# Kernel optimization log

Measured on AMD Instinct MI355X. Metric: run time of the kernel, lower is better.

## Reference

```python
import jax, jax.numpy as jnp
import numpy as np

HIDDEN = 768
HEADS = 12


def setup_inputs() -> dict:
    key = jax.random.key(0)
    ks = jax.random.split(key, 9)
    B, T, C = 2, 4096, HIDDEN
    s = 1.0 / np.sqrt(C)
    x = jax.random.normal(ks[0], (B, T, C), dtype=jnp.float32)
    Wq = jax.random.normal(ks[1], (C, C), dtype=jnp.float32) * s
    bq = jnp.zeros((C,), dtype=jnp.float32)
    Wk = jax.random.normal(ks[2], (C, C), dtype=jnp.float32) * s
    bk = jnp.zeros((C,), dtype=jnp.float32)
    Wv = jax.random.normal(ks[3], (C, C), dtype=jnp.float32) * s
    bv = jnp.zeros((C,), dtype=jnp.float32)
    Wo = jax.random.normal(ks[4], (C, C), dtype=jnp.float32) * s
    bo = jnp.zeros((C,), dtype=jnp.float32)
    return {"x": x, "Wq": Wq, "bq": bq, "Wk": Wk, "bk": bk,
            "Wv": Wv, "bv": bv, "Wo": Wo, "bo": bo}


def reference(x, Wq, bq, Wk, bk, Wv, bv, Wo, bo):
    B, T, C = x.shape
    H = HEADS
    D = C // H
    # projections -> [B, H, T, D]
    def split_heads(y):
        return y.reshape(B, T, H, D).transpose(0, 2, 1, 3)
    q = split_heads(x @ Wq + bq)
    k = split_heads(x @ Wk + bk)
    v = split_heads(x @ Wv + bv)
    # scores [B, H, T, T], scaled by 1/sqrt(D)
    scores = jnp.einsum('bhqd,bhkd->bhqk', q, k) / jnp.sqrt(jnp.asarray(D, x.dtype))
    causal = jnp.tril(jnp.ones((T, T), dtype=bool))
    scores = jnp.where(causal[None, None], scores, jnp.asarray(-jnp.inf, x.dtype))
    weights = jax.nn.softmax(scores, axis=-1)
    # dropout_prob = 0.0 (eval-equivalent), so dropouts are identity
    out = jnp.einsum('bhqk,bhkd->bhqd', weights, v)  # [B,H,T,D]
    out = out.transpose(0, 2, 1, 3).reshape(B, T, C)
    return out @ Wo + bo
```

## Files before the change

kernel.cpp:

```cpp
#include <hip/hip_runtime.h>

typedef unsigned short ushort_t;
typedef __bf16 bf16x8 __attribute__((ext_vector_type(8)));
typedef float f4v __attribute__((ext_vector_type(4)));

#define B_ 2
#define T_ 4096
#define C_ 768
#define H_ 12
#define D_ 64
#define BT_ (B_*T_)

#define XB_SZ   (BT_*C_*2)
#define WT_SZ   (C_*C_*2)
#define QKV_SZ  (BT_*C_*2)
#define WS_XB   0
#define WS_WT   (WS_XB + XB_SZ)
#define WS_Q    (WS_WT + 4*WT_SZ)
#define WS_K    (WS_Q + QKV_SZ)
#define WS_V    (WS_K + QKV_SZ)
#define WS_AO   (WS_V + QKV_SZ)
#define WS_TOTAL (WS_AO + QKV_SZ)

#define QSCALE  0.18033688f

__device__ __forceinline__ ushort_t f2bf(float f) {
    unsigned u = __float_as_uint(f);
    u += 0x7FFFu + ((u >> 16) & 1u);
    return (ushort_t)(u >> 16);
}

__device__ __forceinline__ void gload16(const void* gsrc, void* ldst) {
    __builtin_amdgcn_global_load_lds(
        (const __attribute__((address_space(1))) unsigned int*)gsrc,
        (__attribute__((address_space(3))) unsigned int*)ldst, 16, 0, 0);
}

__global__ __launch_bounds__(256) void k_convert_x(const float* __restrict__ x,
                                                   ushort_t* __restrict__ xb, int n4) {
    int i = blockIdx.x * 256 + threadIdx.x;
    if (i >= n4) return;
    float4 v = ((const float4*)x)[i];
    ushort4 o;
    o.x = f2bf(v.x); o.y = f2bf(v.y); o.z = f2bf(v.z); o.w = f2bf(v.w);
    ((ushort4*)xb)[i] = o;
}

__global__ __launch_bounds__(256) void k_wt(const float* __restrict__ w0,
                                            const float* __restrict__ w1,
                                            const float* __restrict__ w2,
                                            const float* __restrict__ w3,
                                            ushort_t* __restrict__ wt) {
    __shared__ float tile[32][33];
    int wi = blockIdx.z;
    const float* W = (wi == 0) ? w0 : (wi == 1) ? w1 : (wi == 2) ? w2 : w3;
    ushort_t* out = wt + wi * C_ * C_;
    int k0 = blockIdx.x * 32, n0 = blockIdx.y * 32;
    int tx = threadIdx.x & 31, ty = threadIdx.x >> 5;
#pragma unroll
    for (int i = 0; i < 4; ++i) {
        int kr = ty * 4 + i;
        tile[kr][tx] = W[(k0 + kr) * C_ + n0 + tx];
    }
    __syncthreads();
#pragma unroll
    for (int i = 0; i < 4; ++i) {
        int nr = ty * 4 + i;
        out[(n0 + nr) * C_ + k0 + tx] = f2bf(tile[tx][nr]);
    }
}

__global__ __launch_bounds__(256) void k_gemm_qkv(
    const ushort_t* __restrict__ Xb, const ushort_t* __restrict__ WtAll,
    const float* __restrict__ bq, const float* __restrict__ bk, const float* __restrict__ bv,
    ushort_t* __restrict__ Qo, ushort_t* __restrict__ Ko, ushort_t* __restrict__ Vo) {
    __shared__ ushort_t lsA[128 * 64];
    __shared__ ushort_t lsB[128 * 64];
    char* lsAb = (char*)lsA;
    char* lsBb = (char*)lsB;
    const int z = blockIdx.z;
    const ushort_t* Wt = WtAll + z * C_ * C_;
    const float* bias = (z == 0) ? bq : (z == 1) ? bk : bv;
    const int m0 = blockIdx.x * 128, n0 = blockIdx.y * 128;
    const int tid = threadIdx.x;
    const int w = tid >> 6, lane = tid & 63, lg = lane >> 4, lr = lane & 15;
    const int wm = w >> 1, wn = w & 1;
    f4v acc[4][4] = {};
    for (int ks = 0; ks < 12; ++ks) {
        const int k0 = ks * 64;
        __syncthreads();
#pragma unroll
        for (int i = 0; i < 4; ++i) {
            int s = tid + 256 * i;
            int r = s >> 3, cs = (s & 7) ^ (r & 7);
            gload16(Xb + (m0 + r) * C_ + k0 + cs * 8, lsAb + i * 4096 + w * 1024);
            gload16(Wt + (n0 + r) * C_ + k0 + cs * 8, lsBb + i * 4096 + w * 1024);
        }
        __syncthreads();
#pragma unroll
        for (int kk = 0; kk < 2; ++kk) {
            bf16x8 af[4], bfr[4];
            const int kb = (kk * 32 + lg * 8) * 2;
#pragma unroll
            for (int i = 0; i < 4; ++i) {
                int ra = wm * 64 + i * 16 + lr;
                af[i] = *(const bf16x8*)(lsAb + ra * 128 + (kb ^ ((ra & 7) << 4)));
                int rb = wn * 64 + i * 16 + lr;
                bfr[i] = *(const bf16x8*)(lsBb + rb * 128 + (kb ^ ((rb & 7) << 4)));
            }
#pragma unroll
            for (int mi = 0; mi < 4; ++mi)
#pragma unroll
                for (int nj = 0; nj < 4; ++nj)
                    acc[mi][nj] = __builtin_amdgcn_mfma_f32_16x16x32_bf16(af[mi], bfr[nj], acc[mi][nj], 0, 0, 0);
        }
    }
    const float scale = (z == 0) ? QSCALE : 1.0f;
    const int mbase = m0 + wm * 64, nbase = n0 + wn * 64;
    if (z < 2) {
        ushort_t* outp = (z == 0) ? Qo : Ko;
#pragma unroll
        for (int mi = 0; mi < 4; ++mi) {
#pragma unroll
            for (int nj = 0; nj < 4; ++nj) {
                int col = nbase + nj * 16 + lr;
                int h = col >> 6, d = col & 63;
                float bv_ = bias[col];
#pragma unroll
                for (int j = 0; j < 4; ++j) {
                    int m = mbase + mi * 16 + lg * 4 + j;
                    int bb = m >> 12, t = m & 4095;
                    outp[((bb * H_ + h) * T_ + t) * D_ + d] = f2bf((acc[mi][nj][j] + bv_) * scale);
                }
            }
        }
    } else {
#pragma unroll
        for (int mi = 0; mi < 4; ++mi) {
            int m0j = mbase + mi * 16 + lg * 4;
            int bb = m0j >> 12, t0 = m0j & 4095;
#pragma unroll
            for (int nj = 0; nj < 4; ++nj) {
                int col = nbase + nj * 16 + lr;
                int h = col >> 6, d = col & 63;
                float bv_ = bias[col];
                ushort4 pk;
                pk.x = f2bf(acc[mi][nj][0] + bv_);
                pk.y = f2bf(acc[mi][nj][1] + bv_);
                pk.z = f2bf(acc[mi][nj][2] + bv_);
                pk.w = f2bf(acc[mi][nj][3] + bv_);
                *(ushort4*)(Vo + ((size_t)(bb * H_ + h) * D_ + d) * T_ + t0) = pk;
            }
        }
    }
}

__global__ __launch_bounds__(256) void k_flash(const ushort_t* __restrict__ Q,
                                               const ushort_t* __restrict__ K,
                                               const ushort_t* __restrict__ Vt,
                                               ushort_t* __restrict__ AO) {
    __shared__ ushort_t lsK[64 * 64];
    __shared__ ushort_t lsV[64 * 64];
    __shared__ ushort_t lsP[4 * 16 * 64];
    char* lsKb = (char*)lsK;
    char* lsVb = (char*)lsV;
    const int idx = blockIdx.x;
    const int pi = idx / 24;
    const int bh = idx % 24;
    const int b = bh / H_, h = bh % H_;
    const int tid = threadIdx.x, w = tid >> 6, lane = tid & 63, lg = lane >> 4, lr = lane & 15;
    char* lsPb = (char*)(lsP + w * 16 * 64);
    const ushort_t* qb = Q + (size_t)bh * T_ * D_;
    const ushort_t* kb = K + (size_t)bh * T_ * D_;
    const ushort_t* vtb = Vt + (size_t)bh * D_ * T_;
    ushort_t* aob = AO + (size_t)b * T_ * C_ + h * D_;

    for (int half = 0; half < 2; ++half) {
        const int qt = half ? pi : (63 - pi);
        const int q0 = qt * 64;
        const int wave_qmin = q0 + w * 16;
        bf16x8 aq[2];
#pragma unroll
        for (int kk = 0; kk < 2; ++kk)
            aq[kk] = *(const bf16x8*)(qb + (size_t)(wave_qmin + lr) * D_ + kk * 32 + lg * 8);
        float m_s[4], l_s[4];
        f4v o[4] = {};
#pragma unroll
        for (int j = 0; j < 4; ++j) { m_s[j] = -1e30f; l_s[j] = 0.f; }

        const int ntiles = qt + 1;
        for (int kt = 0; kt < ntiles; ++kt) {
            const int kv0 = kt * 64;
            __syncthreads();
#pragma unroll
            for (int i = 0; i < 2; ++i) {
                int s = tid + 256 * i;
                int r = s >> 3, cs = (s & 7) ^ (r & 7);
                gload16(kb + (size_t)(kv0 + r) * D_ + cs * 8, lsKb + i * 4096 + w * 1024);
                gload16(vtb + (size_t)r * T_ + kv0 + cs * 8, lsVb + i * 4096 + w * 1024);
            }
            __syncthreads();
            f4v sf[4] = {};
#pragma unroll
            for (int kk = 0; kk < 2; ++kk) {
                const int kbyte = (kk * 32 + lg * 8) * 2;
                bf16x8 bk_[4];
#pragma unroll
                for (int nt = 0; nt < 4; ++nt) {
                    int rk = nt * 16 + lr;
                    bk_[nt] = *(const bf16x8*)(lsKb + rk * 128 + (kbyte ^ ((rk & 7) << 4)));
                }
                __builtin_amdgcn_s_setprio(1);
#pragma unroll
                for (int nt = 0; nt < 4; ++nt)
                    sf[nt] = __builtin_amdgcn_mfma_f32_16x16x32_bf16(aq[kk], bk_[nt], sf[nt], 0, 0, 0);
                __builtin_amdgcn_s_setprio(0);
            }
            if (kv0 + 63 > wave_qmin) {
#pragma unroll
                for (int nt = 0; nt < 4; ++nt)
#pragma unroll
                    for (int j = 0; j < 4; ++j) {
                        int qg = wave_qmin + lg * 4 + j;
                        int kg = kv0 + nt * 16 + lr;
                        if (kg > qg) sf[nt][j] = -1e30f;
                    }
            }
#pragma unroll
            for (int j = 0; j < 4; ++j) {
                float rm = fmaxf(fmaxf(sf[0][j], sf[1][j]), fmaxf(sf[2][j], sf[3][j]));
                rm = fmaxf(rm, __shfl_xor(rm, 1));
                rm = fmaxf(rm, __shfl_xor(rm, 2));
                rm = fmaxf(rm, __shfl_xor(rm, 4));
                rm = fmaxf(rm, __shfl_xor(rm, 8));
                float mo = m_s[j];
                float mn = fmaxf(mo, rm);
                float alpha = exp2f(mo - mn);
                float rs = 0.f;
                int prow = lg * 4 + j;
#pragma unroll
                for (int nt = 0; nt < 4; ++nt) {
                    float p = exp2f(sf[nt][j] - mn);
                    rs += p;
                    int cbyte = (nt * 16 + lr) * 2;
                    *(ushort_t*)(lsPb + prow * 128 + (cbyte ^ ((prow & 7) << 4))) = f2bf(p);
                }
                rs += __shfl_xor(rs, 1);
                rs += __shfl_xor(rs, 2);
                rs += __shfl_xor(rs, 4);
                rs += __shfl_xor(rs, 8);
                l_s[j] = l_s[j] * alpha + rs;
                m_s[j] = mn;
#pragma unroll
                for (int nt = 0; nt < 4; ++nt) o[nt][j] *= alpha;
            }
#pragma unroll
            for (int kk = 0; kk < 2; ++kk) {
                const int kvbyte = (kk * 32 + lg * 8) * 2;
                bf16x8 ap, bv_[4];
                ap = *(const bf16x8*)(lsPb + lr * 128 + (kvbyte ^ ((lr & 7) << 4)));
#pragma unroll
                for (int nt = 0; nt < 4; ++nt) {
                    int rd = nt * 16 + lr;
                    bv_[nt] = *(const bf16x8*)(lsVb + rd * 128 + (kvbyte ^ ((rd & 7) << 4)));
                }
                __builtin_amdgcn_s_setprio(1);
#pragma unroll
                for (int nt = 0; nt < 4; ++nt)
                    o[nt] = __builtin_amdgcn_mfma_f32_16x16x32_bf16(ap, bv_[nt], o[nt], 0, 0, 0);
                __builtin_amdgcn_s_setprio(0);
            }
        }
#pragma unroll
        for (int j = 0; j < 4; ++j) {
            float inv = 1.f / l_s[j];
            int qg = wave_qmin + lg * 4 + j;
#pragma unroll
            for (int nt = 0; nt < 4; ++nt) {
                int d = nt * 16 + lr;
                aob[(size_t)qg * C_ + d] = f2bf(o[nt][j] * inv);
            }
        }
    }
}

__global__ __launch_bounds__(256) void k_gemm_out(const ushort_t* __restrict__ Ab,
                                                  const ushort_t* __restrict__ Wt,
                                                  const float* __restrict__ bo,
                                                  float* __restrict__ Out) {
    __shared__ ushort_t lsA[128 * 64];
    __shared__ ushort_t lsB[128 * 64];
    char* lsAb = (char*)lsA;
    char* lsBb = (char*)lsB;
    const int m0 = blockIdx.x * 128, n0 = blockIdx.y * 128;
    const int tid = threadIdx.x;
    const int w = tid >> 6, lane = tid & 63, lg = lane >> 4, lr = lane & 15;
    const int wm = w >> 1, wn = w & 1;
    f4v acc[4][4] = {};
    for (int ks = 0; ks < 12; ++ks) {
        const int k0 = ks * 64;
        __syncthreads();
#pragma unroll
        for (int i = 0; i < 4; ++i) {
            int s = tid + 256 * i;
            int r = s >> 3, cs = (s & 7) ^ (r & 7);
            gload16(Ab + (m0 + r) * C_ + k0 + cs * 8, lsAb + i * 4096 + w * 1024);
            gload16(Wt + (n0 + r) * C_ + k0 + cs * 8, lsBb + i * 4096 + w * 1024);
        }
        __syncthreads();
#pragma unroll
        for (int kk = 0; kk < 2; ++kk) {
            bf16x8 af[4], bfr[4];
            const int kb = (kk * 32 + lg * 8) * 2;
#pragma unroll
            for (int i = 0; i < 4; ++i) {
                int ra = wm * 64 + i * 16 + lr;
                af[i] = *(const bf16x8*)(lsAb + ra * 128 + (kb ^ ((ra & 7) << 4)));
                int rb = wn * 64 + i * 16 + lr;
                bfr[i] = *(const bf16x8*)(lsBb + rb * 128 + (kb ^ ((rb & 7) << 4)));
            }
#pragma unroll
            for (int mi = 0; mi < 4; ++mi)
#pragma unroll
                for (int nj = 0; nj < 4; ++nj)
                    acc[mi][nj] = __builtin_amdgcn_mfma_f32_16x16x32_bf16(af[mi], bfr[nj], acc[mi][nj], 0, 0, 0);
        }
    }
    const int mbase = m0 + wm * 64, nbase = n0 + wn * 64;
#pragma unroll
    for (int mi = 0; mi < 4; ++mi) {
#pragma unroll
        for (int nj = 0; nj < 4; ++nj) {
            int col = nbase + nj * 16 + lr;
            float bv_ = bo[col];
#pragma unroll
            for (int j = 0; j < 4; ++j) {
                int m = mbase + mi * 16 + lg * 4 + j;
                Out[(size_t)m * C_ + col] = acc[mi][nj][j] + bv_;
            }
        }
    }
}

extern "C" void kernel_launch(void* const* d_in, const int* in_sizes, int n_in,
                              void* d_out, int out_size, void* d_ws, size_t ws_size,
                              hipStream_t stream) {
    const float* x  = (const float*)d_in[0];
    const float* Wq = (const float*)d_in[1];
    const float* bq = (const float*)d_in[2];
    const float* Wk = (const float*)d_in[3];
    const float* bk = (const float*)d_in[4];
    const float* Wv = (const float*)d_in[5];
    const float* bv = (const float*)d_in[6];
    const float* Wo = (const float*)d_in[7];
    const float* bo = (const float*)d_in[8];
    float* out = (float*)d_out;
    char* ws = (char*)d_ws;
    if (ws_size < (size_t)WS_TOTAL) return;

    ushort_t* Xb = (ushort_t*)(ws + WS_XB);
    ushort_t* Wt = (ushort_t*)(ws + WS_WT);
    ushort_t* Qb = (ushort_t*)(ws + WS_Q);
    ushort_t* Kb = (ushort_t*)(ws + WS_K);
    ushort_t* Vb = (ushort_t*)(ws + WS_V);
    ushort_t* Ao = (ushort_t*)(ws + WS_AO);

    k_convert_x<<<dim3(BT_ * C_ / 4 / 256), 256, 0, stream>>>(x, Xb, BT_ * C_ / 4);
    k_wt<<<dim3(24, 24, 4), 256, 0, stream>>>(Wq, Wk, Wv, Wo, Wt);
    k_gemm_qkv<<<dim3(64, 6, 3), 256, 0, stream>>>(Xb, Wt, bq, bk, bv, Qb, Kb, Vb);
    k_flash<<<dim3(32 * 24), 256, 0, stream>>>(Qb, Kb, Vb, Ao);
    k_gemm_out<<<dim3(64, 6), 256, 0, stream>>>(Ao, Wt + 3 * C_ * C_, bo, out);
}
```

Measured before the change: 342.9 us.

## Restructure flash attention to 2-wave blocks with 32 query rows per wave and transposed scores

The flash kernel now launches one 128-thread block per 64-row query tile instead of pairing two tiles in a 256-thread block. Each wave handles 32 query rows across two 16-row fragments, so every K/V fragment loaded from LDS feeds twice as many MFMAs. The score product is computed transposed (K as the A operand), which makes the row max and sum reductions mostly lane-local and lets P be written to LDS as packed bf16 pairs. It also uses raw v_exp_f32, and drops the s_setprio hints. The trade-offs are more blocks with uneven causal work that are no longer load-balanced in pairs, and more registers per wave.

New measurement: 289.8 us. -15.5%, faster.

```diff
diff --git a/kernel.cpp b/kernel.cpp
--- a/kernel.cpp
+++ b/kernel.cpp
@@ -1,4 +1,5 @@
 #include <hip/hip_runtime.h>
+#include <hip/hip_bf16.h>
 
 typedef unsigned short ushort_t;
 typedef __bf16 bf16x8 __attribute__((ext_vector_type(8)));
@@ -28,6 +29,17 @@
     unsigned u = __float_as_uint(f);
     u += 0x7FFFu + ((u >> 16) & 1u);
     return (ushort_t)(u >> 16);
+}
+
+__device__ __forceinline__ float ex2(float x) {
+    float r;
+    asm("v_exp_f32 %0, %1" : "=v"(r) : "v"(x));
+    return r;
+}
+
+__device__ __forceinline__ unsigned pk2bf(float a, float b) {
+    __hip_bfloat162 h = __float22bfloat162_rn(float2{a, b});
+    return *reinterpret_cast<unsigned*>(&h);
 }
 
 __device__ __forceinline__ void gload16(const void* gsrc, void* ldst) {
@@ -155,132 +167,150 @@
     }
 }
 
-__global__ __launch_bounds__(256) void k_flash(const ushort_t* __restrict__ Q,
-                                               const ushort_t* __restrict__ K,
-                                               const ushort_t* __restrict__ Vt,
-                                               ushort_t* __restrict__ AO) {
+__global__ __launch_bounds__(128, 3) void k_flash(const ushort_t* __restrict__ Q,
+                                                  const ushort_t* __restrict__ K,
+                                                  const ushort_t* __restrict__ Vt,
+                                                  ushort_t* __restrict__ AO) {
     __shared__ ushort_t lsK[64 * 64];
     __shared__ ushort_t lsV[64 * 64];
-    __shared__ ushort_t lsP[4 * 16 * 64];
+    __shared__ ushort_t lsP[2 * 32 * 64];
     char* lsKb = (char*)lsK;
     char* lsVb = (char*)lsV;
     const int idx = blockIdx.x;
-    const int pi = idx / 24;
+    const int qt = 63 - idx / 24;
     const int bh = idx % 24;
     const int b = bh / H_, h = bh % H_;
+    const int q0 = qt * 64;
     const int tid = threadIdx.x, w = tid >> 6, lane = tid & 63, lg = lane >> 4, lr = lane & 15;
-    char* lsPb = (char*)(lsP + w * 16 * 64);
+    char* lsPb = (char*)(lsP + w * 32 * 64);
     const ushort_t* qb = Q + (size_t)bh * T_ * D_;
     const ushort_t* kb = K + (size_t)bh * T_ * D_;
     const ushort_t* vtb = Vt + (size_t)bh * D_ * T_;
     ushort_t* aob = AO + (size_t)b * T_ * C_ + h * D_;
-
-    for (int half = 0; half < 2; ++half) {
-        const int qt = half ? pi : (63 - pi);
-        const int q0 = qt * 64;
-        const int wave_qmin = q0 + w * 16;
-        bf16x8 aq[2];
+    const int wave_qmin = q0 + w * 32;
+
+    bf16x8 aq[2][2];
+#pragma unroll
+    for (int qf = 0; qf < 2; ++qf)
 #pragma unroll
         for (int kk = 0; kk < 2; ++kk)
-            aq[kk] = *(const bf16x8*)(qb + (size_t)(wave_qmin + lr) * D_ + kk * 32 + lg * 8);
-        float m_s[4], l_s[4];
-        f4v o[4] = {};
-#pragma unroll
-        for (int j = 0; j < 4; ++j) { m_s[j] = -1e30f; l_s[j] = 0.f; }
-
-        const int ntiles = qt + 1;
-        for (int kt = 0; kt < ntiles; ++kt) {
-            const int kv0 = kt * 64;
-            __syncthreads();
-#pragma unroll
-            for (int i = 0; i < 2; ++i) {
-                int s = tid + 256 * i;
-                int r = s >> 3, cs = (s & 7) ^ (r & 7);
-                gload16(kb + (size_t)(kv0 + r) * D_ + cs * 8, lsKb + i * 4096 + w * 1024);
-                gload16(vtb + (size_t)r * T_ + kv0 + cs * 8, lsVb + i * 4096 + w * 1024);
-            }
-            __syncthreads();
-            f4v sf[4] = {};
-#pragma unroll
-            for (int kk = 0; kk < 2; ++kk) {
-                const int kbyte = (kk * 32 + lg * 8) * 2;
-                bf16x8 bk_[4];
-#pragma unroll
-                for (int nt = 0; nt < 4; ++nt) {
-                    int rk = nt * 16 + lr;
-                    bk_[nt] = *(const bf16x8*)(lsKb + rk * 128 + (kbyte ^ ((rk & 7) << 4)));
-                }
-                __builtin_amdgcn_s_setprio(1);
+            aq[qf][kk] = *(const bf16x8*)(qb + (size_t)(wave_qmin + qf * 16 + lr) * D_ + kk * 32 + lg * 8);
+
+    float m_s[2] = {-1e30f, -1e30f};
+    float l_s[2] = {0.f, 0.f};
+    f4v o[2][4] = {};
+
+    const int ntiles = qt + 1;
+    for (int kt = 0; kt < ntiles; ++kt) {
+        const int kv0 = kt * 64;
+        __syncthreads();
+#pragma unroll
+        for (int i = 0; i < 4; ++i) {
+            int s = tid + 128 * i;
+            int r = s >> 3, cs = (s & 7) ^ (r & 7);
+            gload16(kb + (size_t)(kv0 + r) * D_ + cs * 8, lsKb + i * 2048 + w * 1024);
+            gload16(vtb + (size_t)r * T_ + kv0 + cs * 8, lsVb + i * 2048 + w * 1024);
+        }
+        __syncthreads();
+
+        f4v sfT[2][4] = {};
+#pragma unroll
+        for (int kk = 0; kk < 2; ++kk) {
+            const int kbyte = (kk * 32 + lg * 8) * 2;
+            bf16x8 bk_[4];
+#pragma unroll
+            for (int nt = 0; nt < 4; ++nt) {
+                int rk = nt * 16 + lr;
+                bk_[nt] = *(const bf16x8*)(lsKb + rk * 128 + (kbyte ^ ((rk & 7) << 4)));
+            }
+#pragma unroll
+            for (int qf = 0; qf < 2; ++qf)
 #pragma unroll
                 for (int nt = 0; nt < 4; ++nt)
-                    sf[nt] = __builtin_amdgcn_mfma_f32_16x16x32_bf16(aq[kk], bk_[nt], sf[nt], 0, 0, 0);
-                __builtin_amdgcn_s_setprio(0);
-            }
-            if (kv0 + 63 > wave_qmin) {
+                    sfT[qf][nt] = __builtin_amdgcn_mfma_f32_16x16x32_bf16(bk_[nt], aq[qf][kk], sfT[qf][nt], 0, 0, 0);
+        }
+        if (kv0 + 63 > wave_qmin) {
+#pragma unroll
+            for (int qf = 0; qf < 2; ++qf) {
+                int qg = wave_qmin + qf * 16 + lr;
 #pragma unroll
                 for (int nt = 0; nt < 4; ++nt)
 #pragma unroll
                     for (int j = 0; j < 4; ++j) {
-                        int qg = wave_qmin + lg * 4 + j;
-                        int kg = kv0 + nt * 16 + lr;
-                        if (kg > qg) sf[nt][j] = -1e30f;
+                        int kg = kv0 + nt * 16 + lg * 4 + j;
+                        if (kg > qg) sfT[qf][nt][j] = -1e30f;
                     }
             }
+        }
+#pragma unroll
+        for (int qf = 0; qf < 2; ++qf) {
+            float rm = -1e30f;
+#pragma unroll
+            for (int nt = 0; nt < 4; ++nt)
+#pragma unroll
+                for (int j = 0; j < 4; ++j) rm = fmaxf(rm, sfT[qf][nt][j]);
+            rm = fmaxf(rm, __shfl_xor(rm, 16));
+            rm = fmaxf(rm, __shfl_xor(rm, 32));
+            float mo = m_s[qf];
+            float mn = fmaxf(mo, rm);
+            float al = ex2(mo - mn);
+            float rs = 0.f;
+            const int prow = qf * 16 + lr;
+            const int pswz = (prow & 7) << 4;
+#pragma unroll
+            for (int nt = 0; nt < 4; ++nt) {
+                float p0 = ex2(sfT[qf][nt][0] - mn);
+                float p1 = ex2(sfT[qf][nt][1] - mn);
+                float p2 = ex2(sfT[qf][nt][2] - mn);
+                float p3 = ex2(sfT[qf][nt][3] - mn);
+                rs += (p0 + p1) + (p2 + p3);
+                uint2 pk;
+                pk.x = pk2bf(p0, p1);
+                pk.y = pk2bf(p2, p3);
+                *(uint2*)(lsPb + prow * 128 + ((nt * 32 + lg * 8) ^ pswz)) = pk;
+            }
+            rs += __shfl_xor(rs, 16);
+            rs += __shfl_xor(rs, 32);
+            l_s[qf] = l_s[qf] * al + rs;
+            m_s[qf] = mn;
+#pragma unroll
+            for (int nt = 0; nt < 4; ++nt)
+#pragma unroll
+                for (int j = 0; j < 4; ++j) o[qf][nt][j] *= al;
+        }
+#pragma unroll
+        for (int kk = 0; kk < 2; ++kk) {
+            const int kvbyte = (kk * 32 + lg * 8) * 2;
+            bf16x8 bv_[4], ap[2];
+#pragma unroll
+            for (int nt = 0; nt < 4; ++nt) {
+                int rd = nt * 16 + lr;
+                bv_[nt] = *(const bf16x8*)(lsVb + rd * 128 + (kvbyte ^ ((rd & 7) << 4)));
+            }
+#pragma unroll
+            for (int qf = 0; qf < 2; ++qf) {
+                int rp = qf * 16 + lr;
+                ap[qf] = *(const bf16x8*)(lsPb + rp * 128 + (kvbyte ^ ((rp & 7) << 4)));
+            }
+#pragma unroll
+            for (int qf = 0; qf < 2; ++qf)
+#pragma unroll
+                for (int nt = 0; nt < 4; ++nt)
+                    o[qf][nt] = __builtin_amdgcn_mfma_f32_16x16x32_bf16(bv_[nt], ap[qf], o[qf][nt], 0, 0, 0);
+        }
+    }
+#pragma unroll
+    for (int qf = 0; qf < 2; ++qf) {
+        float inv = 1.f / l_s[qf];
+        int qg = wave_qmin + qf * 16 + lr;
+        ushort_t* orow = aob + (size_t)qg * C_;
+#pragma unroll
+        for (int nt = 0; nt < 4; ++nt)
 #pragma unroll
             for (int j = 0; j < 4; ++j) {
-                float rm = fmaxf(fmaxf(sf[0][j], sf[1][j]), fmaxf(sf[2][j], sf[3][j]));
-                rm = fmaxf(rm, __shfl_xor(rm, 1));
-                rm = fmaxf(rm, __shfl_xor(rm, 2));
-                rm = fmaxf(rm, __shfl_xor(rm, 4));
-                rm = fmaxf(rm, __shfl_xor(rm, 8));
-                float mo = m_s[j];
-                float mn = fmaxf(mo, rm);
-                float alpha = exp2f(mo - mn);
-                float rs = 0.f;
-                int prow = lg * 4 + j;
-#pragma unroll
-                for (int nt = 0; nt < 4; ++nt) {
-                    float p = exp2f(sf[nt][j] - mn);
-                    rs += p;
-                    int cbyte = (nt * 16 + lr) * 2;
-                    *(ushort_t*)(lsPb + prow * 128 + (cbyte ^ ((prow & 7) << 4))) = f2bf(p);
-                }
-                rs += __shfl_xor(rs, 1);
-                rs += __shfl_xor(rs, 2);
-                rs += __shfl_xor(rs, 4);
-                rs += __shfl_xor(rs, 8);
-                l_s[j] = l_s[j] * alpha + rs;
-                m_s[j] = mn;
-#pragma unroll
-                for (int nt = 0; nt < 4; ++nt) o[nt][j] *= alpha;
-            }
-#pragma unroll
-            for (int kk = 0; kk < 2; ++kk) {
-                const int kvbyte = (kk * 32 + lg * 8) * 2;
-                bf16x8 ap, bv_[4];
-                ap = *(const bf16x8*)(lsPb + lr * 128 + (kvbyte ^ ((lr & 7) << 4)));
-#pragma unroll
-                for (int nt = 0; nt < 4; ++nt) {
-                    int rd = nt * 16 + lr;
-                    bv_[nt] = *(const bf16x8*)(lsVb + rd * 128 + (kvbyte ^ ((rd & 7) << 4)));
-                }
-                __builtin_amdgcn_s_setprio(1);
-#pragma unroll
-                for (int nt = 0; nt < 4; ++nt)
-                    o[nt] = __builtin_amdgcn_mfma_f32_16x16x32_bf16(ap, bv_[nt], o[nt], 0, 0, 0);
-                __builtin_amdgcn_s_setprio(0);
-            }
-        }
-#pragma unroll
-        for (int j = 0; j < 4; ++j) {
-            float inv = 1.f / l_s[j];
-            int qg = wave_qmin + lg * 4 + j;
-#pragma unroll
-            for (int nt = 0; nt < 4; ++nt) {
-                int d = nt * 16 + lr;
-                aob[(size_t)qg * C_ + d] = f2bf(o[nt][j] * inv);
-            }
-        }
+                int d = nt * 16 + lg * 4 + j;
+                orow[d] = f2bf(o[qf][nt][j] * inv);
+            }
     }
 }
 
@@ -368,6 +398,6 @@
     k_convert_x<<<dim3(BT_ * C_ / 4 / 256), 256, 0, stream>>>(x, Xb, BT_ * C_ / 4);
     k_wt<<<dim3(24, 24, 4), 256, 0, stream>>>(Wq, Wk, Wv, Wo, Wt);
     k_gemm_qkv<<<dim3(64, 6, 3), 256, 0, stream>>>(Xb, Wt, bq, bk, bv, Qb, Kb, Vb);
-    k_flash<<<dim3(32 * 24), 256, 0, stream>>>(Qb, Kb, Vb, Ao);
+    k_flash<<<dim3(64 * 24), 128, 0, stream>>>(Qb, Kb, Vb, Ao);
     k_gemm_out<<<dim3(64, 6), 256, 0, stream>>>(Ao, Wt + 3 * C_ * C_, bo, out);
 }
```

## Rewrite flash attention with 32x32 MFMA, register-resident P, double-buffered K/V

Applied to the files above, without the earlier changes.

The flash kernel now computes S transposed with 32x32x16 MFMAs, so each lane owns one query row and the row max/sum need a single cross-half shuffle. P stays in registers, packed with v_cvt_pk_bf16_f32 and v_permlane32_swap, instead of a round trip through LDS. K/V tiles are double-buffered so the next tile's loads overlap compute. The launch changes to 128-thread blocks with one query tile each, replacing the paired long/short tile balancing, which risks tail imbalance across the causal workload.

Result: faster. 284.7 us (-17.0%).

```diff
diff --git a/kernel.cpp b/kernel.cpp
--- a/kernel.cpp
+++ b/kernel.cpp
@@ -1,8 +1,10 @@
 #include <hip/hip_runtime.h>
+#include <hip/hip_bf16.h>
 
 typedef unsigned short ushort_t;
 typedef __bf16 bf16x8 __attribute__((ext_vector_type(8)));
 typedef float f4v __attribute__((ext_vector_type(4)));
+typedef float f16v __attribute__((ext_vector_type(16)));
 
 #define B_ 2
 #define T_ 4096
@@ -28,6 +30,18 @@
     unsigned u = __float_as_uint(f);
     u += 0x7FFFu + ((u >> 16) & 1u);
     return (ushort_t)(u >> 16);
+}
+
+__device__ __forceinline__ float ex2(float x) {
+    float r;
+    asm("v_exp_f32 %0, %1" : "=v"(r) : "v"(x));
+    return r;
+}
+
+__device__ __forceinline__ unsigned cvtpk(float a, float b) {
+    unsigned r;
+    asm("v_cvt_pk_bf16_f32 %0, %1, %2" : "=v"(r) : "v"(a), "v"(b));
+    return r;
 }
 
 __device__ __forceinline__ void gload16(const void* gsrc, void* ldst) {
@@ -155,133 +169,146 @@
     }
 }
 
-__global__ __launch_bounds__(256) void k_flash(const ushort_t* __restrict__ Q,
+__global__ __launch_bounds__(128) void k_flash(const ushort_t* __restrict__ Q,
                                                const ushort_t* __restrict__ K,
                                                const ushort_t* __restrict__ Vt,
                                                ushort_t* __restrict__ AO) {
-    __shared__ ushort_t lsK[64 * 64];
-    __shared__ ushort_t lsV[64 * 64];
-    __shared__ ushort_t lsP[4 * 16 * 64];
-    char* lsKb = (char*)lsK;
-    char* lsVb = (char*)lsV;
+    __shared__ ushort_t lsK[2][64 * 64];
+    __shared__ ushort_t lsV[2][64 * 64];
     const int idx = blockIdx.x;
-    const int pi = idx / 24;
+    const int qt = 63 - idx / 24;
     const int bh = idx % 24;
     const int b = bh / H_, h = bh % H_;
-    const int tid = threadIdx.x, w = tid >> 6, lane = tid & 63, lg = lane >> 4, lr = lane & 15;
-    char* lsPb = (char*)(lsP + w * 16 * 64);
+    const int q0 = qt * 64;
+    const int tid = threadIdx.x, w = tid >> 6;
+    const int lane = tid & 63, l31 = lane & 31, hf = lane >> 5;
     const ushort_t* qb = Q + (size_t)bh * T_ * D_;
     const ushort_t* kb = K + (size_t)bh * T_ * D_;
     const ushort_t* vtb = Vt + (size_t)bh * D_ * T_;
-    ushort_t* aob = AO + (size_t)b * T_ * C_ + h * D_;
-
-    for (int half = 0; half < 2; ++half) {
-        const int qt = half ? pi : (63 - pi);
-        const int q0 = qt * 64;
-        const int wave_qmin = q0 + w * 16;
-        bf16x8 aq[2];
-#pragma unroll
-        for (int kk = 0; kk < 2; ++kk)
-            aq[kk] = *(const bf16x8*)(qb + (size_t)(wave_qmin + lr) * D_ + kk * 32 + lg * 8);
-        float m_s[4], l_s[4];
-        f4v o[4] = {};
-#pragma unroll
-        for (int j = 0; j < 4; ++j) { m_s[j] = -1e30f; l_s[j] = 0.f; }
-
-        const int ntiles = qt + 1;
-        for (int kt = 0; kt < ntiles; ++kt) {
-            const int kv0 = kt * 64;
-            __syncthreads();
-#pragma unroll
-            for (int i = 0; i < 2; ++i) {
-                int s = tid + 256 * i;
-                int r = s >> 3, cs = (s & 7) ^ (r & 7);
-                gload16(kb + (size_t)(kv0 + r) * D_ + cs * 8, lsKb + i * 4096 + w * 1024);
-                gload16(vtb + (size_t)r * T_ + kv0 + cs * 8, lsVb + i * 4096 + w * 1024);
-            }
-            __syncthreads();
-            f4v sf[4] = {};
-#pragma unroll
-            for (int kk = 0; kk < 2; ++kk) {
-                const int kbyte = (kk * 32 + lg * 8) * 2;
-                bf16x8 bk_[4];
-#pragma unroll
-                for (int nt = 0; nt < 4; ++nt) {
-                    int rk = nt * 16 + lr;
-                    bk_[nt] = *(const bf16x8*)(lsKb + rk * 128 + (kbyte ^ ((rk & 7) << 4)));
+    const int qw = q0 + w * 32;
+    const int myq = qw + l31;
+
+    bf16x8 aq[4];
+#pragma unroll
+    for (int c = 0; c < 4; ++c)
+        aq[c] = *(const bf16x8*)(qb + (size_t)myq * D_ + c * 16 + hf * 8);
+
+    float m_s = -1e30f, l_s = 0.f;
+    f16v o[2] = {};
+
+    const int ntiles = qt + 1;
+
+#define STAGE(bufi, kt_) do {                                                   \
+        const int kv0s = (kt_) * 64;                                            \
+        char* dK = (char*)lsK[bufi];                                            \
+        char* dV = (char*)lsV[bufi];                                            \
+        _Pragma("unroll")                                                       \
+        for (int i_ = 0; i_ < 4; ++i_) {                                        \
+            int s_ = tid + 128 * i_;                                            \
+            int r_ = s_ >> 3, cs_ = (s_ & 7) ^ (r_ & 7);                        \
+            gload16(kb + (size_t)(kv0s + r_) * D_ + cs_ * 8, dK + i_ * 2048 + w * 1024); \
+            gload16(vtb + (size_t)r_ * T_ + kv0s + cs_ * 8, dV + i_ * 2048 + w * 1024);  \
+        }                                                                       \
+    } while (0)
+
+    STAGE(0, 0);
+    __syncthreads();
+
+    for (int kt = 0; kt < ntiles; ++kt) {
+        const int cur = kt & 1;
+        if (kt + 1 < ntiles) STAGE(cur ^ 1, kt + 1);
+        const char* sK = (const char*)lsK[cur];
+        const char* sV = (const char*)lsV[cur];
+        const int kv0 = kt * 64;
+
+        f16v sT[2] = {};
+#pragma unroll
+        for (int kb_ = 0; kb_ < 2; ++kb_) {
+            const int row = kb_ * 32 + l31;
+            const int swz = (row & 7) << 4;
+#pragma unroll
+            for (int c = 0; c < 4; ++c) {
+                bf16x8 ak = *(const bf16x8*)(sK + row * 128 + ((c * 32 + hf * 16) ^ swz));
+                sT[kb_] = __builtin_amdgcn_mfma_f32_32x32x16_bf16(ak, aq[c], sT[kb_], 0, 0, 0);
+            }
+        }
+        if (kv0 + 63 > qw) {
+#pragma unroll
+            for (int kb_ = 0; kb_ < 2; ++kb_)
+#pragma unroll
+                for (int r = 0; r < 16; ++r) {
+                    int kv = kv0 + kb_ * 32 + (r & 3) + 8 * (r >> 2) + 4 * hf;
+                    if (kv > myq) sT[kb_][r] = -1e30f;
                 }
-                __builtin_amdgcn_s_setprio(1);
-#pragma unroll
-                for (int nt = 0; nt < 4; ++nt)
-                    sf[nt] = __builtin_amdgcn_mfma_f32_16x16x32_bf16(aq[kk], bk_[nt], sf[nt], 0, 0, 0);
-                __builtin_amdgcn_s_setprio(0);
-            }
-            if (kv0 + 63 > wave_qmin) {
-#pragma unroll
-                for (int nt = 0; nt < 4; ++nt)
-#pragma unroll
-                    for (int j = 0; j < 4; ++j) {
-                        int qg = wave_qmin + lg * 4 + j;
-                        int kg = kv0 + nt * 16 + lr;
-                        if (kg > qg) sf[nt][j] = -1e30f;
-                    }
-            }
-#pragma unroll
-            for (int j = 0; j < 4; ++j) {
-                float rm = fmaxf(fmaxf(sf[0][j], sf[1][j]), fmaxf(sf[2][j], sf[3][j]));
-                rm = fmaxf(rm, __shfl_xor(rm, 1));
-                rm = fmaxf(rm, __shfl_xor(rm, 2));
-                rm = fmaxf(rm, __shfl_xor(rm, 4));
-                rm = fmaxf(rm, __shfl_xor(rm, 8));
-                float mo = m_s[j];
-                float mn = fmaxf(mo, rm);
-                float alpha = exp2f(mo - mn);
-                float rs = 0.f;
-                int prow = lg * 4 + j;
-#pragma unroll
-                for (int nt = 0; nt < 4; ++nt) {
-                    float p = exp2f(sf[nt][j] - mn);
-                    rs += p;
-                    int cbyte = (nt * 16 + lr) * 2;
-                    *(ushort_t*)(lsPb + prow * 128 + (cbyte ^ ((prow & 7) << 4))) = f2bf(p);
-                }
-                rs += __shfl_xor(rs, 1);
-                rs += __shfl_xor(rs, 2);
-                rs += __shfl_xor(rs, 4);
-                rs += __shfl_xor(rs, 8);
-                l_s[j] = l_s[j] * alpha + rs;
-                m_s[j] = mn;
-#pragma unroll
-                for (int nt = 0; nt < 4; ++nt) o[nt][j] *= alpha;
-            }
-#pragma unroll
-            for (int kk = 0; kk < 2; ++kk) {
-                const int kvbyte = (kk * 32 + lg * 8) * 2;
-                bf16x8 ap, bv_[4];
-                ap = *(const bf16x8*)(lsPb + lr * 128 + (kvbyte ^ ((lr & 7) << 4)));
-#pragma unroll
-                for (int nt = 0; nt < 4; ++nt) {
-                    int rd = nt * 16 + lr;
-                    bv_[nt] = *(const bf16x8*)(lsVb + rd * 128 + (kvbyte ^ ((rd & 7) << 4)));
-                }
-                __builtin_amdgcn_s_setprio(1);
-#pragma unroll
-                for (int nt = 0; nt < 4; ++nt)
-                    o[nt] = __builtin_amdgcn_mfma_f32_16x16x32_bf16(ap, bv_[nt], o[nt], 0, 0, 0);
-                __builtin_amdgcn_s_setprio(0);
-            }
-        }
-#pragma unroll
-        for (int j = 0; j < 4; ++j) {
-            float inv = 1.f / l_s[j];
-            int qg = wave_qmin + lg * 4 + j;
-#pragma unroll
-            for (int nt = 0; nt < 4; ++nt) {
-                int d = nt * 16 + lr;
-                aob[(size_t)qg * C_ + d] = f2bf(o[nt][j] * inv);
-            }
-        }
-    }
+        }
+        float rm = -1e30f;
+#pragma unroll
+        for (int kb_ = 0; kb_ < 2; ++kb_)
+#pragma unroll
+            for (int r = 0; r < 16; ++r) rm = fmaxf(rm, sT[kb_][r]);
+        rm = fmaxf(rm, __shfl_xor(rm, 32));
+        const float mn = fmaxf(m_s, rm);
+        const float al = ex2(m_s - mn);
+        float rs = 0.f;
+#pragma unroll
+        for (int kb_ = 0; kb_ < 2; ++kb_)
+#pragma unroll
+            for (int r = 0; r < 16; ++r) {
+                float p = ex2(sT[kb_][r] - mn);
+                sT[kb_][r] = p;
+                rs += p;
+            }
+        rs += __shfl_xor(rs, 32);
+        l_s = l_s * al + rs;
+        m_s = mn;
+#pragma unroll
+        for (int db = 0; db < 2; ++db)
+#pragma unroll
+            for (int r = 0; r < 16; ++r) o[db][r] *= al;
+
+        unsigned pb[4][4];
+#pragma unroll
+        for (int kb_ = 0; kb_ < 2; ++kb_) {
+#pragma unroll
+            for (int cc = 0; cc < 2; ++cc) {
+                const int rb = cc * 8;
+                unsigned a0 = cvtpk(sT[kb_][rb + 0], sT[kb_][rb + 1]);
+                unsigned b0 = cvtpk(sT[kb_][rb + 4], sT[kb_][rb + 5]);
+                unsigned a1 = cvtpk(sT[kb_][rb + 2], sT[kb_][rb + 3]);
+                unsigned b1 = cvtpk(sT[kb_][rb + 6], sT[kb_][rb + 7]);
+                asm("v_permlane32_swap_b32 %0, %1" : "+v"(a0), "+v"(b0));
+                asm("v_permlane32_swap_b32 %0, %1" : "+v"(a1), "+v"(b1));
+                const int c16 = kb_ * 2 + cc;
+                pb[c16][0] = a0; pb[c16][1] = a1; pb[c16][2] = b0; pb[c16][3] = b1;
+            }
+        }
+#pragma unroll
+        for (int db = 0; db < 2; ++db) {
+            const int row = db * 32 + l31;
+            const int swz = (row & 7) << 4;
+#pragma unroll
+            for (int c16 = 0; c16 < 4; ++c16) {
+                bf16x8 av = *(const bf16x8*)(sV + row * 128 + ((c16 * 32 + hf * 16) ^ swz));
+                o[db] = __builtin_amdgcn_mfma_f32_32x32x16_bf16(av, *(const bf16x8*)&pb[c16][0], o[db], 0, 0, 0);
+            }
+        }
+        __syncthreads();
+    }
+#undef STAGE
+
+    const float inv = 1.f / l_s;
+    ushort_t* orow = AO + ((size_t)b * T_ + myq) * C_ + h * D_;
+#pragma unroll
+    for (int db = 0; db < 2; ++db)
+#pragma unroll
+        for (int g = 0; g < 4; ++g) {
+            ushort4 pk;
+            pk.x = f2bf(o[db][g * 4 + 0] * inv);
+            pk.y = f2bf(o[db][g * 4 + 1] * inv);
+            pk.z = f2bf(o[db][g * 4 + 2] * inv);
+            pk.w = f2bf(o[db][g * 4 + 3] * inv);
+            *(ushort4*)(orow + db * 32 + g * 8 + hf * 4) = pk;
+        }
 }
 
 __global__ __launch_bounds__(256) void k_gemm_out(const ushort_t* __restrict__ Ab,
@@ -368,6 +395,6 @@
     k_convert_x<<<dim3(BT_ * C_ / 4 / 256), 256, 0, stream>>>(x, Xb, BT_ * C_ / 4);
     k_wt<<<dim3(24, 24, 4), 256, 0, stream>>>(Wq, Wk, Wv, Wo, Wt);
     k_gemm_qkv<<<dim3(64, 6, 3), 256, 0, stream>>>(Xb, Wt, bq, bk, bv, Qb, Kb, Vb);
-    k_flash<<<dim3(32 * 24), 256, 0, stream>>>(Qb, Kb, Vb, Ao);
+    k_flash<<<dim3(64 * 24), 128, 0, stream>>>(Qb, Kb, Vb, Ao);
     k_gemm_out<<<dim3(64, 6), 256, 0, stream>>>(Ao, Wt + 3 * C_ * C_, bo, out);
 }
```
